# Performance work log

Hardware: AMD Instinct MI355X
Metric: run time of the kernel (lower is better)

The kernel has to match this reference:

```python
import jax, jax.numpy as jnp
import numpy as np

N_NODES = 50000
N_EDGES = 1600000
IN_DIM = 128
HID = 64
HEADS = 4
N_GRAPHS = 64
OUT_DIM = 10
NEG_SLOPE = 0.2  # PyG GATConv default leaky_relu slope


def _glorot(key, shape):
    fan_in = shape[0] if len(shape) > 1 else shape[-1]
    return jax.random.normal(key, shape, dtype=jnp.float32) / np.sqrt(fan_in)


def setup_inputs() -> dict:
    key = jax.random.key(0)
    ks = jax.random.split(key, 24)
    imgs = jax.random.normal(ks[0], (N_NODES, IN_DIM), dtype=jnp.float32)
    edge_index = jax.random.randint(ks[1], (2, N_EDGES), 0, N_NODES, dtype=jnp.int32)
    batch = jnp.sort(jax.random.randint(ks[2], (N_NODES,), 0, N_GRAPHS, dtype=jnp.int32))
    HC = HID * HEADS
    inp = {
        'imgs': imgs, 'edge_index': edge_index, 'batch': batch,
        # superpixel aggregator: Linear(input_dim, hidden)
        'W_agg': _glorot(ks[3], (IN_DIM, HID)), 'b_agg': jnp.zeros((HID,), jnp.float32),
        # GAT layer 0: hidden -> heads*hidden, concat
        'W0': _glorot(ks[4], (HID, HC)), 'as0': _glorot(ks[5], (HEADS, HID)), 'ad0': _glorot(ks[6], (HEADS, HID)), 'b0': jnp.zeros((HC,), jnp.float32),
        # GAT layer 1: heads*hidden -> heads*hidden, concat
        'W1': _glorot(ks[7], (HC, HC)), 'as1': _glorot(ks[8], (HEADS, HID)), 'ad1': _glorot(ks[9], (HEADS, HID)), 'b1': jnp.zeros((HC,), jnp.float32),
        # GAT layer 2: heads*hidden -> hidden, mean over heads
        'W2': _glorot(ks[10], (HC, HC)), 'as2': _glorot(ks[11], (HEADS, HID)), 'ad2': _glorot(ks[12], (HEADS, HID)), 'b2': jnp.zeros((HID,), jnp.float32),
        # MLP: hidden -> hidden -> out
        'mW1': _glorot(ks[13], (HID, HID)), 'mb1': jnp.zeros((HID,), jnp.float32),
        'mW2': _glorot(ks[14], (HID, OUT_DIM)), 'mb2': jnp.zeros((OUT_DIM,), jnp.float32),
    }
    return inp


def _gat_conv(x, src, dst, W, a_src, a_dst, b, concat):
    # PyG GATConv: linear -> per-head scores -> leaky_relu -> segment softmax over dst -> scatter-add
    N = x.shape[0]
    H, C = a_src.shape
    h = (x @ W).reshape(N, H, C)                      # [N,H,C]
    es = jnp.sum(h * a_src, axis=-1)                  # [N,H]
    ed = jnp.sum(h * a_dst, axis=-1)                  # [N,H]
    e = jax.nn.leaky_relu(es[src] + ed[dst], NEG_SLOPE)  # [E,H]
    m = jax.ops.segment_max(e, dst, num_segments=N)
    m = jnp.where(jnp.isfinite(m), m, 0.0)
    ex = jnp.exp(e - m[dst])                          # [E,H]
    s = jax.ops.segment_sum(ex, dst, num_segments=N)
    alpha = ex / (s[dst] + 1e-16)                     # [E,H]
    out = jax.ops.segment_sum(h[src] * alpha[..., None], dst, num_segments=N)  # [N,H,C]
    out = out.reshape(N, H * C) if concat else out.mean(axis=1)
    return out + b


def _forward(imgs, edge_index, batch, W_agg, b_agg, W0, as0, ad0, b0, W1, as1, ad1, b1, W2, as2, ad2, b2, mW1, mb1, mW2, mb2):
    N = imgs.shape[0]
    # add self loops (PyG GATConv default add_self_loops=True)
    loop = jnp.arange(N, dtype=edge_index.dtype)
    src = jnp.concatenate([edge_index[0], loop])
    dst = jnp.concatenate([edge_index[1], loop])
    x = imgs @ W_agg + b_agg                          # lrgb aggregator
    x = jax.nn.elu(_gat_conv(x, src, dst, W0, as0, ad0, b0, True))
    x = jax.nn.elu(_gat_conv(x, src, dst, W1, as1, ad1, b1, True))
    x = _gat_conv(x, src, dst, W2, as2, ad2, b2, False)
    # global mean pool over graphs
    sums = jax.ops.segment_sum(x, batch, num_segments=N_GRAPHS)
    cnt = jax.ops.segment_sum(jnp.ones((N,), x.dtype), batch, num_segments=N_GRAPHS)
    pooled = sums / jnp.maximum(cnt, 1.0)[:, None]
    # MLP (dropout inactive at inference)
    hmlp = jax.nn.relu(pooled @ mW1 + mb1)
    return hmlp @ mW2 + mb2


def reference(imgs, edge_index, batch, W_agg, b_agg, W0, as0, ad0, b0, W1, as1, ad1, b1, W2, as2, ad2, b2, mW1, mb1, mW2, mb2):
    return _forward(imgs, edge_index, batch, W_agg, b_agg, W0, as0, ad0, b0, W1, as1, ad1, b1, W2, as2, ad2, b2, mW1, mb1, mW2, mb2)
```

## Files before the change

kernel.cpp:

```cpp
#include <hip/hip_runtime.h>
#include <hip/hip_bf16.h>

#define N_NODES 50000
#define N_EDGESX 1600000
#define E_TOT   (N_EDGESX + N_NODES)
#define IN_DIM 128
#define HID 64
#define HEADS 4
#define HC 256
#define N_GRAPHS 64
#define OUT_DIM 10
#define NEG_SLOPE 0.2f

#define NBUK 196
#define CAP 12288
#define BT 4096

typedef __attribute__((ext_vector_type(8))) short bf16x8;
typedef __attribute__((ext_vector_type(4))) float f32x4;

__device__ __forceinline__ float lrelu(float x){ return fmaxf(x, NEG_SLOPE*x); }
__device__ __forceinline__ float sel4(float4 v, int i){
  float r = v.x;
  r = (i==1) ? v.y : r;
  r = (i==2) ? v.z : r;
  r = (i==3) ? v.w : r;
  return r;
}
__device__ __forceinline__ unsigned short f2bf(float f){
  union { __hip_bfloat16 b; unsigned short u; } cv;
  cv.b = __float2bfloat16(f);
  return cv.u;
}
__device__ __forceinline__ float bflo(unsigned int u){ return __uint_as_float(u << 16); }
__device__ __forceinline__ float bfhi(unsigned int u){ return __uint_as_float(u & 0xffff0000u); }

__global__ __launch_bounds__(256) void bin_k(const int* __restrict__ ei,
                                             int* __restrict__ bucket_cursor,
                                             unsigned int* __restrict__ bucket_buf){
  __shared__ unsigned int pk[BT];
  __shared__ unsigned int binned[BT];
  __shared__ int hist[256], excl[256], gbase[256], lcur[256], tmp[256];
  const int tid = threadIdx.x;
  const int e0 = blockIdx.x * BT;
  const int nv = min(BT, E_TOT - e0);
  hist[tid] = 0;
  __syncthreads();
  for (int i = tid; i < nv; i += 256){
    int e = e0 + i;
    int src, dst;
    if (e < N_EDGESX){ src = ei[e]; dst = ei[N_EDGESX + e]; }
    else { src = e - N_EDGESX; dst = src; }
    pk[i] = ((unsigned)src << 16) | (unsigned)dst;
    atomicAdd(&hist[dst >> 8], 1);
  }
  __syncthreads();
  int v = hist[tid];
  tmp[tid] = v;
  __syncthreads();
  for (int off = 1; off < 256; off <<= 1){
    int t = (tid >= off) ? tmp[tid-off] : 0;
    __syncthreads();
    tmp[tid] += t;
    __syncthreads();
  }
  excl[tid] = tmp[tid] - v;
  lcur[tid] = tmp[tid] - v;
  if (tid < NBUK && v > 0) gbase[tid] = atomicAdd(&bucket_cursor[tid], v);
  __syncthreads();
  for (int i = tid; i < nv; i += 256){
    unsigned u = pk[i];
    int b = (int)((u & 0xFFFFu) >> 8);
    int p = atomicAdd(&lcur[b], 1);
    binned[p] = u;
  }
  __syncthreads();
  for (int j = tid; j < nv; j += 256){
    unsigned u = binned[j];
    int b = (int)((u & 0xFFFFu) >> 8);
    bucket_buf[(size_t)b*CAP + gbase[b] + (j - excl[b])] = u;
  }
}

__global__ __launch_bounds__(256) void bucket_scan_k(const int* __restrict__ bucket_cursor,
                                                     int* __restrict__ bucket_base,
                                                     int* __restrict__ row_start){
  __shared__ int tmp[256];
  int t = threadIdx.x;
  int v = (t < NBUK) ? bucket_cursor[t] : 0;
  tmp[t] = v;
  __syncthreads();
  for (int off = 1; off < 256; off <<= 1){
    int x = (t >= off) ? tmp[t-off] : 0;
    __syncthreads();
    tmp[t] += x;
    __syncthreads();
  }
  if (t < NBUK) bucket_base[t] = tmp[t] - v;
  if (t == 0) row_start[N_NODES] = E_TOT;
}

__global__ __launch_bounds__(256) void build_k(const unsigned int* __restrict__ bucket_buf,
                                               const int* __restrict__ bucket_cursor,
                                               const int* __restrict__ bucket_base,
                                               int* __restrict__ row_start,
                                               int* __restrict__ csr_src){
  __shared__ int hist[256], excl[256], lcur[256], tmp[256];
  const int b = blockIdx.x;
  const int t = threadIdx.x;
  const int cntb = bucket_cursor[b];
  const int base = bucket_base[b];
  const unsigned int* buf = bucket_buf + (size_t)b*CAP;
  hist[t] = 0;
  __syncthreads();
  for (int i = t; i < cntb; i += 256) atomicAdd(&hist[buf[i] & 255], 1);
  __syncthreads();
  int v = hist[t];
  tmp[t] = v;
  __syncthreads();
  for (int off = 1; off < 256; off <<= 1){
    int x = (t >= off) ? tmp[t-off] : 0;
    __syncthreads();
    tmp[t] += x;
    __syncthreads();
  }
  excl[t] = tmp[t] - v;
  lcur[t] = tmp[t] - v;
  int g = b*256 + t;
  if (g < N_NODES) row_start[g] = base + excl[t];
  __syncthreads();
  for (int i = t; i < cntb; i += 256){
    unsigned u = buf[i];
    int p = atomicAdd(&lcur[u & 255], 1);
    csr_src[base + p] = (int)(u >> 16);
  }
}

__global__ __launch_bounds__(256) void wcvt_k(const float* __restrict__ W, unsigned short* __restrict__ WT, int K){
  int idx = blockIdx.x*256 + threadIdx.x;
  if (idx >= K*256) return;
  int k = idx >> 8, c = idx & 255;
  WT[c*K + k] = f2bf(W[k*256 + c]);
}

__global__ __launch_bounds__(256) void wproj_k(const float* __restrict__ W0,
    const float* __restrict__ as0, const float* __restrict__ ad0,
    float* __restrict__ ws0, float* __restrict__ wd0){
  int t = threadIdx.x;
  int h = t >> 6, k = t & 63;
  float s = 0.f, d = 0.f;
  for (int c = 0; c < 64; c++){
    float wv = W0[k*256 + h*64 + c];
    s = fmaf(wv, as0[h*64 + c], s);
    d = fmaf(wv, ad0[h*64 + c], d);
  }
  ws0[t] = s; wd0[t] = d;
}

__global__ __launch_bounds__(256) void agg_lin(const float* __restrict__ imgs, const float* __restrict__ W,
                                               const float* __restrict__ b,
                                               const float* __restrict__ ws0, const float* __restrict__ wd0,
                                               unsigned short* __restrict__ x0,
                                               float* __restrict__ es, float* __restrict__ ed){
  __shared__ __align__(16) float xr[4][IN_DIM];
  int w = threadIdx.x >> 6, lane = threadIdx.x & 63;
  int n = blockIdx.x*4 + w;
  if (n >= N_NODES) return;
  ((float2*)xr[w])[lane] = ((const float2*)(imgs + (size_t)n*IN_DIM))[lane];
  float acc = b[lane];
  #pragma unroll 8
  for (int k = 0; k < IN_DIM; k++)
    acc = fmaf(xr[w][k], W[k*HID + lane], acc);
  x0[(size_t)n*HID + lane] = f2bf(acc);
  float p[4], q[4];
  #pragma unroll
  for (int h = 0; h < 4; h++){
    p[h] = acc * ws0[h*64 + lane];
    q[h] = acc * wd0[h*64 + lane];
  }
  #pragma unroll
  for (int off = 32; off >= 1; off >>= 1){
    #pragma unroll
    for (int h = 0; h < 4; h++){
      p[h] += __shfl_xor(p[h], off);
      q[h] += __shfl_xor(q[h], off);
    }
  }
  if (lane == 0){
    float4 pv; pv.x=p[0]; pv.y=p[1]; pv.z=p[2]; pv.w=p[3];
    float4 qv; qv.x=q[0]; qv.y=q[1]; qv.z=q[2]; qv.w=q[3];
    *(float4*)(es + n*4) = pv;
    *(float4*)(ed + n*4) = qv;
  }
}

__global__ __launch_bounds__(256) void gat_agg0(const unsigned short* __restrict__ x0,
    const float* __restrict__ es, const float* __restrict__ ed,
    const int* __restrict__ row_start, const int* __restrict__ csr_src,
    unsigned short* __restrict__ y4){
  __shared__ int   sbuf[4][64];
  __shared__ float wbuf[4][64][4];
  const int lane = threadIdx.x & 63;
  const int wid  = threadIdx.x >> 6;
  const int n = blockIdx.x*4 + wid;
  if (n >= N_NODES) return;
  const int rs = row_start[n], re = row_start[n+1];
  const float4 edn = *(const float4*)(ed + n*4);
  const int slot = lane >> 3;
  const int f8   = lane & 7;
  float4 sumw = make_float4(0.f,0.f,0.f,0.f);
  float acc[4][8];
  #pragma unroll
  for (int h=0;h<4;h++)
    #pragma unroll
    for (int q2=0;q2<8;q2++) acc[h][q2]=0.f;

  for (int base = rs; base < re; base += 64){
    const int cl = min(64, re - base);
    int e = base + lane;
    int s = (e < re) ? csr_src[e] : 0;
    float4 e4 = *(const float4*)(es + (s<<2));
    float w0 = __expf(lrelu(e4.x + edn.x));
    float w1 = __expf(lrelu(e4.y + edn.y));
    float w2 = __expf(lrelu(e4.z + edn.z));
    float w3 = __expf(lrelu(e4.w + edn.w));
    if (e >= re){ w0=0.f; w1=0.f; w2=0.f; w3=0.f; }
    sumw.x += w0; sumw.y += w1; sumw.z += w2; sumw.w += w3;
    sbuf[wid][lane] = s;
    float4 wv; wv.x=w0; wv.y=w1; wv.z=w2; wv.w=w3;
    *(float4*)wbuf[wid][lane] = wv;
    for (int j = 0; j < cl; j += 8){
      int jj = j + slot;
      if (jj < cl){
        float4 aw = *(const float4*)wbuf[wid][jj];
        int s2 = sbuf[wid][jj];
        uint4 hv = *(const uint4*)(x0 + (((size_t)s2)<<6) + (f8<<3));
        float f[8] = {bflo(hv.x),bfhi(hv.x),bflo(hv.y),bfhi(hv.y),
                      bflo(hv.z),bfhi(hv.z),bflo(hv.w),bfhi(hv.w)};
        #pragma unroll
        for (int q2=0;q2<8;q2++){
          acc[0][q2] = fmaf(aw.x, f[q2], acc[0][q2]);
          acc[1][q2] = fmaf(aw.y, f[q2], acc[1][q2]);
          acc[2][q2] = fmaf(aw.z, f[q2], acc[2][q2]);
          acc[3][q2] = fmaf(aw.w, f[q2], acc[3][q2]);
        }
      }
    }
  }
  #pragma unroll
  for (int off = 8; off <= 32; off <<= 1){
    #pragma unroll
    for (int h=0;h<4;h++)
      #pragma unroll
      for (int q2=0;q2<8;q2++) acc[h][q2] += __shfl_xor(acc[h][q2], off);
  }
  #pragma unroll
  for (int off = 32; off >= 1; off >>= 1){
    sumw.x += __shfl_xor(sumw.x, off);
    sumw.y += __shfl_xor(sumw.y, off);
    sumw.z += __shfl_xor(sumw.z, off);
    sumw.w += __shfl_xor(sumw.w, off);
  }
  if (lane < 32){
    int h = lane >> 3;
    float inv = 1.f / (sel4(sumw, h) + 1e-16f);
    union { unsigned short u[8]; uint4 v; } ob;
    #pragma unroll
    for (int q2=0;q2<8;q2++) ob.u[q2] = f2bf(acc[h][q2] * inv);
    *(uint4*)(y4 + (size_t)n*HC + lane*8) = ob.v;
  }
}

__global__ __launch_bounds__(256) void hgemm_k(const unsigned short* __restrict__ y4,
                                               const unsigned short* __restrict__ WT0,
                                               const float* __restrict__ b0,
                                               unsigned short* __restrict__ x1){
  __shared__ __align__(16) unsigned short xs[16][264];
  const int tid = threadIdx.x;
  const int lane = tid & 63;
  const int w = tid >> 6;
  const int n0 = blockIdx.x * 16;
  for (int i = tid; i < 16*32; i += 256){
    int r = i >> 5, cc = (i & 31) * 8;
    *(uint4*)(&xs[r][cc]) = *(const uint4*)(y4 + (size_t)(n0+r)*HC + cc);
  }
  __syncthreads();
  const int g = lane >> 4, cl = lane & 15;
  f32x4 acc[4];
  #pragma unroll
  for (int c = 0; c < 4; c++) acc[c] = (f32x4){0.f,0.f,0.f,0.f};
  #pragma unroll
  for (int t = 0; t < 2; t++){
    bf16x8 a = *(const bf16x8*)(&xs[cl][w*64 + t*32 + g*8]);
    #pragma unroll
    for (int c = 0; c < 4; c++){
      bf16x8 bv = *(const bf16x8*)(WT0 + (size_t)(w*64 + c*16 + cl)*64 + t*32 + g*8);
      acc[c] = __builtin_amdgcn_mfma_f32_16x16x32_bf16(a, bv, acc[c], 0, 0, 0);
    }
  }
  #pragma unroll
  for (int c = 0; c < 4; c++){
    int col = w*64 + c*16 + cl;
    float bb = b0[col];
    #pragma unroll
    for (int j = 0; j < 4; j++){
      float v = acc[c][j] + bb;
      v = v > 0.f ? v : expm1f(v);
      x1[(size_t)(n0 + g*4 + j)*HC + col] = f2bf(v);
    }
  }
}

template<int K>
__global__ __launch_bounds__(256) void lin_mfma(const unsigned short* __restrict__ x,
                                                const unsigned short* __restrict__ WT,
                                                const float* __restrict__ as_, const float* __restrict__ ad_,
                                                unsigned short* __restrict__ hh,
                                                float* __restrict__ es, float* __restrict__ ed){
  constexpr int KP = K + 8;
  __shared__ __align__(16) unsigned short xs[16][KP];
  const int tid = threadIdx.x;
  const int lane = tid & 63;
  const int w = tid >> 6;
  const int n0 = blockIdx.x * 16;
  constexpr int CH = K/8;
  for (int i = tid; i < 16*CH; i += 256){
    int r = i / CH, cc = (i % CH)*8;
    *(uint4*)(&xs[r][cc]) = *(const uint4*)(x + (size_t)(n0+r)*K + cc);
  }
  __syncthreads();
  const int g  = lane >> 4;
  const int cl = lane & 15;
  f32x4 acc[4];
  #pragma unroll
  for (int c = 0; c < 4; c++) acc[c] = (f32x4){0.f,0.f,0.f,0.f};
  #pragma unroll
  for (int t = 0; t < K/32; t++){
    bf16x8 a = *(const bf16x8*)(&xs[cl][t*32 + g*8]);
    #pragma unroll
    for (int c = 0; c < 4; c++){
      bf16x8 bv = *(const bf16x8*)(WT + (size_t)(w*64 + c*16 + cl)*K + t*32 + g*8);
      acc[c] = __builtin_amdgcn_mfma_f32_16x16x32_bf16(a, bv, acc[c], 0, 0, 0);
    }
  }
  float pes[4] = {0.f,0.f,0.f,0.f}, ped[4] = {0.f,0.f,0.f,0.f};
  #pragma unroll
  for (int c = 0; c < 4; c++){
    float av = as_[w*64 + c*16 + cl];
    float dv = ad_[w*64 + c*16 + cl];
    #pragma unroll
    for (int j = 0; j < 4; j++){
      pes[j] = fmaf(acc[c][j], av, pes[j]);
      ped[j] = fmaf(acc[c][j], dv, ped[j]);
    }
  }
  #pragma unroll
  for (int off = 8; off >= 1; off >>= 1){
    #pragma unroll
    for (int j = 0; j < 4; j++){
      pes[j] += __shfl_xor(pes[j], off);
      ped[j] += __shfl_xor(ped[j], off);
    }
  }
  if (cl == 0){
    #pragma unroll
    for (int j = 0; j < 4; j++){
      int n = n0 + g*4 + j;
      es[n*4 + w] = pes[j];
      ed[n*4 + w] = ped[j];
    }
  }
  #pragma unroll
  for (int c = 0; c < 4; c++){
    #pragma unroll
    for (int j = 0; j < 4; j++){
      hh[((size_t)w*N_NODES + (n0 + g*4 + j))*HID + c*16 + cl] = f2bf(acc[c][j]);
    }
  }
}

template<int ACT, int OBF>
__global__ __launch_bounds__(256) void gat_agg_h(const unsigned short* __restrict__ hh,
    const float* __restrict__ es, const float* __restrict__ ed,
    const int* __restrict__ row_start, const int* __restrict__ csr_src,
    const float* __restrict__ bias, void* __restrict__ outp){
  __shared__ int   sbuf[4][64];
  __shared__ float wbuf[4][64];
  const int lane = threadIdx.x & 63;
  const int wid  = threadIdx.x >> 6;
  const int hy   = blockIdx.y;
  const int n = blockIdx.x*4 + wid;
  if (n >= N_NODES) return;
  const int rs = row_start[n], re = row_start[n+1];
  const float edh = ed[n*4 + hy];
  const int slot = lane >> 3;
  const int f8   = lane & 7;
  const unsigned short* __restrict__ tab = hh + (((size_t)hy * N_NODES) << 6);
  float sumw = 0.f;
  float acc[8];
  #pragma unroll
  for (int q2=0;q2<8;q2++) acc[q2]=0.f;

  for (int base = rs; base < re; base += 64){
    const int cl = min(64, re - base);
    int e = base + lane;
    int s = (e < re) ? csr_src[e] : 0;
    float w = (e < re) ? __expf(lrelu(es[(s<<2)+hy] + edh)) : 0.f;
    sumw += w;
    sbuf[wid][lane] = s;
    wbuf[wid][lane] = w;
    for (int j = 0; j < cl; j += 8){
      int jj = j + slot;
      if (jj < cl){
        float a = wbuf[wid][jj];
        int s2 = sbuf[wid][jj];
        uint4 hv = *(const uint4*)(tab + (((size_t)s2)<<6) + (f8<<3));
        acc[0] = fmaf(a, bflo(hv.x), acc[0]);
        acc[1] = fmaf(a, bfhi(hv.x), acc[1]);
        acc[2] = fmaf(a, bflo(hv.y), acc[2]);
        acc[3] = fmaf(a, bfhi(hv.y), acc[3]);
        acc[4] = fmaf(a, bflo(hv.z), acc[4]);
        acc[5] = fmaf(a, bfhi(hv.z), acc[5]);
        acc[6] = fmaf(a, bflo(hv.w), acc[6]);
        acc[7] = fmaf(a, bfhi(hv.w), acc[7]);
      }
    }
  }
  #pragma unroll
  for (int off = 8; off <= 32; off <<= 1){
    #pragma unroll
    for (int q2=0;q2<8;q2++) acc[q2] += __shfl_xor(acc[q2], off);
  }
  #pragma unroll
  for (int off = 32; off >= 1; off >>= 1) sumw += __shfl_xor(sumw, off);
  const float inv = 1.f / (sumw + 1e-16f);
  float o[8];
  #pragma unroll
  for (int q2=0;q2<8;q2++) o[q2] = acc[q2]*inv;
  if (ACT){
    #pragma unroll
    for (int q2=0;q2<8;q2++){
      float v = o[q2] + bias[hy*64 + f8*8 + q2];
      o[q2] = v > 0.f ? v : expm1f(v);
    }
  }
  if (lane < 8){
    if (OBF){
      union { unsigned short u[8]; uint4 v; } ob;
      #pragma unroll
      for (int q2=0;q2<8;q2++) ob.u[q2] = f2bf(o[q2]);
      *(uint4*)((unsigned short*)outp + (size_t)n*HC + hy*64 + lane*8) = ob.v;
    } else {
      float* dst = (float*)outp + (size_t)n*HC + hy*64 + lane*8;
      float4 v0; v0.x=o[0]; v0.y=o[1]; v0.z=o[2]; v0.w=o[3];
      float4 v1; v1.x=o[4]; v1.y=o[5]; v1.z=o[6]; v1.w=o[7];
      *(float4*)dst = v0;
      *(float4*)(dst+4) = v1;
    }
  }
}

#define PB_NODES 128
__global__ __launch_bounds__(256) void pool_k(const float* __restrict__ xagg,
                                              const int* __restrict__ batch, float* __restrict__ pooled,
                                              float* __restrict__ cnt){
  int c = threadIdx.x & 63;
  int sub = threadIdx.x >> 6;
  int n0 = blockIdx.x * PB_NODES;
  int nend = n0 + PB_NODES; if (nend > N_NODES) nend = N_NODES;
  float acc = 0.f; int curg = -1; int cl = 0;
  for (int n = n0 + sub; n < nend; n += 4){
    int g = batch[n];
    if (g != curg){
      if (curg >= 0){
        unsafeAtomicAdd(pooled + curg*HID + c, acc);
        if (c == 0) unsafeAtomicAdd(cnt + curg, (float)cl);
      }
      curg = g; acc = 0.f; cl = 0;
    }
    const float* r = xagg + (size_t)n*HC;
    acc += 0.25f*(r[c] + r[64+c] + r[128+c] + r[192+c]);
    cl++;
  }
  if (curg >= 0){
    unsafeAtomicAdd(pooled + curg*HID + c, acc);
    if (c == 0) unsafeAtomicAdd(cnt + curg, (float)cl);
  }
}

__global__ __launch_bounds__(64) void mlp_k(const float* __restrict__ pooled, const float* __restrict__ cnt,
                                            const float* __restrict__ b2,
                                            const float* __restrict__ mW1, const float* __restrict__ mb1,
                                            const float* __restrict__ mW2, const float* __restrict__ mb2,
                                            float* __restrict__ out){
  __shared__ float p[HID], h1[HID];
  int g = blockIdx.x, j = threadIdx.x;
  float c = fmaxf(cnt[g], 1.f);
  p[j] = pooled[g*HID + j] / c + b2[j];
  __syncthreads();
  float acc = mb1[j];
  #pragma unroll 8
  for (int k = 0; k < HID; k++) acc = fmaf(p[k], mW1[k*HID + j], acc);
  h1[j] = fmaxf(acc, 0.f);
  __syncthreads();
  if (j < OUT_DIM){
    float a2 = mb2[j];
    #pragma unroll 8
    for (int k = 0; k < HID; k++) a2 = fmaf(h1[k], mW2[k*OUT_DIM + j], a2);
    out[g*OUT_DIM + j] = a2;
  }
}

extern "C" void kernel_launch(void* const* d_in, const int* in_sizes, int n_in,
                              void* d_out, int out_size, void* d_ws, size_t ws_size,
                              hipStream_t stream){
  const float* imgs  = (const float*)d_in[0];
  const int*   ei    = (const int*)d_in[1];
  const int*   batch = (const int*)d_in[2];
  const float* W_agg = (const float*)d_in[3];
  const float* b_agg = (const float*)d_in[4];
  const float* W0 = (const float*)d_in[5];
  const float* as0 = (const float*)d_in[6];
  const float* ad0 = (const float*)d_in[7];
  const float* b0 = (const float*)d_in[8];
  const float* W1 = (const float*)d_in[9];
  const float* as1 = (const float*)d_in[10];
  const float* ad1 = (const float*)d_in[11];
  const float* b1 = (const float*)d_in[12];
  const float* W2 = (const float*)d_in[13];
  const float* as2 = (const float*)d_in[14];
  const float* ad2 = (const float*)d_in[15];
  const float* b2 = (const float*)d_in[16];
  const float* mW1 = (const float*)d_in[17];
  const float* mb1 = (const float*)d_in[18];
  const float* mW2 = (const float*)d_in[19];
  const float* mb2 = (const float*)d_in[20];
  float* out = (float*)d_out;

  float* xf32 = (float*)d_ws;
  unsigned short* y4 = (unsigned short*)xf32;
  unsigned short* hb  = (unsigned short*)(xf32 + (size_t)N_NODES*HC);
  unsigned short* xbf = hb + (size_t)N_NODES*HC;
  float* es   = (float*)(xbf + (size_t)N_NODES*HC);
  float* ed   = es + (size_t)N_NODES*HEADS;
  float* pooled = ed + (size_t)N_NODES*HEADS;
  float* cnt  = pooled + N_GRAPHS*HID;
  float* ws0  = cnt + N_GRAPHS;
  float* wd0  = ws0 + 256;
  int* row_start = (int*)(wd0 + 256);
  int* csr_src   = row_start + (N_NODES+1);
  int* bucket_cursor = csr_src + E_TOT;
  int* bucket_base   = bucket_cursor + NBUK;
  unsigned short* WT0 = (unsigned short*)(bucket_base + NBUK);
  unsigned short* WT1 = WT0 + 256*64;
  unsigned short* WT2 = WT1 + 256*256;
  unsigned int* bucket_buf = (unsigned int*)(WT2 + 256*256);
  unsigned short* x0bf = (unsigned short*)bucket_buf;

  hipMemsetAsync(bucket_cursor, 0, NBUK*sizeof(int), stream);
  bin_k<<<(E_TOT + BT - 1)/BT, 256, 0, stream>>>(ei, bucket_cursor, bucket_buf);
  bucket_scan_k<<<1, 256, 0, stream>>>(bucket_cursor, bucket_base, row_start);
  build_k<<<NBUK, 256, 0, stream>>>(bucket_buf, bucket_cursor, bucket_base, row_start, csr_src);

  wcvt_k<<<(64*256+255)/256, 256, 0, stream>>>(W0, WT0, 64);
  wcvt_k<<<(256*256+255)/256, 256, 0, stream>>>(W1, WT1, 256);
  wcvt_k<<<(256*256+255)/256, 256, 0, stream>>>(W2, WT2, 256);
  wproj_k<<<1, 256, 0, stream>>>(W0, as0, ad0, ws0, wd0);

  const int MB = N_NODES/16;
  const int GB = (N_NODES + 3)/4;
  dim3 GH(GB, HEADS, 1);

  agg_lin<<<GB, 256, 0, stream>>>(imgs, W_agg, b_agg, ws0, wd0, x0bf, es, ed);

  gat_agg0<<<GB, 256, 0, stream>>>(x0bf, es, ed, row_start, csr_src, y4);
  hgemm_k<<<MB, 256, 0, stream>>>(y4, WT0, b0, xbf);

  lin_mfma<256><<<MB, 256, 0, stream>>>(xbf, WT1, as1, ad1, hb, es, ed);
  gat_agg_h<1,1><<<GH, 256, 0, stream>>>(hb, es, ed, row_start, csr_src, b1, xbf);

  lin_mfma<256><<<MB, 256, 0, stream>>>(xbf, WT2, as2, ad2, hb, es, ed);
  gat_agg_h<0,0><<<GH, 256, 0, stream>>>(hb, es, ed, row_start, csr_src, nullptr, xf32);

  hipMemsetAsync(pooled, 0, (N_GRAPHS*HID + N_GRAPHS)*sizeof(float), stream);
  pool_k<<<(N_NODES + PB_NODES - 1)/PB_NODES, 256, 0, stream>>>(xf32, batch, pooled, cnt);
  mlp_k<<<N_GRAPHS, 64, 0, stream>>>(pooled, cnt, b2, mW1, mb1, mW2, mb2, out);
}
```

Measured before the change: 678.1 us.

## Fuse per-head GAT aggregation into one node-major pass over all heads

The projected features move from a head-major layout ([head][node][64]) to a node-major layout ([node][256]). The aggregation kernel now processes all four heads in one wave per destination node instead of launching one block row per head. Each source row is read as one contiguous 512-byte chunk, and the CSR index and attention-score work per edge is done once instead of four times. Address arithmetic switches to 32-bit unsigned offsets. In exchange, each lane does more loads per edge iteration, and the gather footprint per edge is larger.

```diff
diff --git a/kernel.cpp b/kernel.cpp
--- a/kernel.cpp
+++ b/kernel.cpp
@@ -234,7 +234,7 @@
       if (jj < cl){
         float4 aw = *(const float4*)wbuf[wid][jj];
         int s2 = sbuf[wid][jj];
-        uint4 hv = *(const uint4*)(x0 + (((size_t)s2)<<6) + (f8<<3));
+        uint4 hv = *(const uint4*)(x0 + ((unsigned)(s2<<6) + (unsigned)(f8<<3)));
         float f[8] = {bflo(hv.x),bfhi(hv.x),bflo(hv.y),bfhi(hv.y),
                       bflo(hv.z),bfhi(hv.z),bflo(hv.w),bfhi(hv.w)};
         #pragma unroll
@@ -315,7 +315,7 @@
 __global__ __launch_bounds__(256) void lin_mfma(const unsigned short* __restrict__ x,
                                                 const unsigned short* __restrict__ WT,
                                                 const float* __restrict__ as_, const float* __restrict__ ad_,
-                                                unsigned short* __restrict__ hh,
+                                                unsigned short* __restrict__ h,
                                                 float* __restrict__ es, float* __restrict__ ed){
   constexpr int KP = K + 8;
   __shared__ __align__(16) unsigned short xs[16][KP];
@@ -374,89 +374,93 @@
   for (int c = 0; c < 4; c++){
     #pragma unroll
     for (int j = 0; j < 4; j++){
-      hh[((size_t)w*N_NODES + (n0 + g*4 + j))*HID + c*16 + cl] = f2bf(acc[c][j]);
+      h[(size_t)(n0 + g*4 + j)*HC + w*64 + c*16 + cl] = f2bf(acc[c][j]);
     }
   }
 }
 
 template<int ACT, int OBF>
-__global__ __launch_bounds__(256) void gat_agg_h(const unsigned short* __restrict__ hh,
+__global__ __launch_bounds__(256) void gat_agg(const unsigned short* __restrict__ h,
     const float* __restrict__ es, const float* __restrict__ ed,
     const int* __restrict__ row_start, const int* __restrict__ csr_src,
     const float* __restrict__ bias, void* __restrict__ outp){
   __shared__ int   sbuf[4][64];
-  __shared__ float wbuf[4][64];
+  __shared__ float wbuf[4][64][4];
   const int lane = threadIdx.x & 63;
   const int wid  = threadIdx.x >> 6;
-  const int hy   = blockIdx.y;
   const int n = blockIdx.x*4 + wid;
   if (n >= N_NODES) return;
   const int rs = row_start[n], re = row_start[n+1];
-  const float edh = ed[n*4 + hy];
-  const int slot = lane >> 3;
-  const int f8   = lane & 7;
-  const unsigned short* __restrict__ tab = hh + (((size_t)hy * N_NODES) << 6);
-  float sumw = 0.f;
-  float acc[8];
-  #pragma unroll
-  for (int q2=0;q2<8;q2++) acc[q2]=0.f;
+  const float4 edn = *(const float4*)(ed + n*4);
+  const int half = lane >> 5;
+  const int l5   = lane & 31;
+  const int hh   = l5 >> 3;
+  const unsigned voff_lane = (unsigned)(l5 << 3);
+
+  float4 sum4 = make_float4(0.f,0.f,0.f,0.f);
+  float a0=0.f,a1=0.f,a2=0.f,a3=0.f,a4=0.f,a5=0.f,a6=0.f,a7=0.f;
 
   for (int base = rs; base < re; base += 64){
     const int cl = min(64, re - base);
     int e = base + lane;
     int s = (e < re) ? csr_src[e] : 0;
-    float w = (e < re) ? __expf(lrelu(es[(s<<2)+hy] + edh)) : 0.f;
-    sumw += w;
+    float4 e4 = *(const float4*)(es + (s<<2));
+    float w0 = __expf(lrelu(e4.x + edn.x));
+    float w1 = __expf(lrelu(e4.y + edn.y));
+    float w2 = __expf(lrelu(e4.z + edn.z));
+    float w3 = __expf(lrelu(e4.w + edn.w));
+    if (e >= re){ w0=0.f; w1=0.f; w2=0.f; w3=0.f; }
+    sum4.x += w0; sum4.y += w1; sum4.z += w2; sum4.w += w3;
     sbuf[wid][lane] = s;
-    wbuf[wid][lane] = w;
-    for (int j = 0; j < cl; j += 8){
-      int jj = j + slot;
-      if (jj < cl){
-        float a = wbuf[wid][jj];
-        int s2 = sbuf[wid][jj];
-        uint4 hv = *(const uint4*)(tab + (((size_t)s2)<<6) + (f8<<3));
-        acc[0] = fmaf(a, bflo(hv.x), acc[0]);
-        acc[1] = fmaf(a, bfhi(hv.x), acc[1]);
-        acc[2] = fmaf(a, bflo(hv.y), acc[2]);
-        acc[3] = fmaf(a, bfhi(hv.y), acc[3]);
-        acc[4] = fmaf(a, bflo(hv.z), acc[4]);
-        acc[5] = fmaf(a, bfhi(hv.z), acc[5]);
-        acc[6] = fmaf(a, bflo(hv.w), acc[6]);
-        acc[7] = fmaf(a, bfhi(hv.w), acc[7]);
-      }
-    }
-  }
-  #pragma unroll
-  for (int off = 8; off <= 32; off <<= 1){
-    #pragma unroll
-    for (int q2=0;q2<8;q2++) acc[q2] += __shfl_xor(acc[q2], off);
-  }
-  #pragma unroll
-  for (int off = 32; off >= 1; off >>= 1) sumw += __shfl_xor(sumw, off);
-  const float inv = 1.f / (sumw + 1e-16f);
-  float o[8];
-  #pragma unroll
-  for (int q2=0;q2<8;q2++) o[q2] = acc[q2]*inv;
+    float4 wv4; wv4.x=w0; wv4.y=w1; wv4.z=w2; wv4.w=w3;
+    *(float4*)wbuf[wid][lane] = wv4;
+    for (int j = 0; j < cl; j += 2){
+      int jj = j + half;
+      float a  = wbuf[wid][jj][hh];
+      int   s2 = sbuf[wid][jj];
+      uint4 hv = *(const uint4*)(h + ((unsigned)(s2<<8) + voff_lane));
+      a0 = fmaf(a, bflo(hv.x), a0);
+      a1 = fmaf(a, bfhi(hv.x), a1);
+      a2 = fmaf(a, bflo(hv.y), a2);
+      a3 = fmaf(a, bfhi(hv.y), a3);
+      a4 = fmaf(a, bflo(hv.z), a4);
+      a5 = fmaf(a, bfhi(hv.z), a5);
+      a6 = fmaf(a, bflo(hv.w), a6);
+      a7 = fmaf(a, bfhi(hv.w), a7);
+    }
+  }
+  #pragma unroll
+  for (int off = 32; off >= 1; off >>= 1){
+    sum4.x += __shfl_xor(sum4.x, off);
+    sum4.y += __shfl_xor(sum4.y, off);
+    sum4.z += __shfl_xor(sum4.z, off);
+    sum4.w += __shfl_xor(sum4.w, off);
+  }
+  const float inv = 1.f / (sel4(sum4, hh) + 1e-16f);
+  a0 += __shfl_xor(a0, 32); a1 += __shfl_xor(a1, 32);
+  a2 += __shfl_xor(a2, 32); a3 += __shfl_xor(a3, 32);
+  a4 += __shfl_xor(a4, 32); a5 += __shfl_xor(a5, 32);
+  a6 += __shfl_xor(a6, 32); a7 += __shfl_xor(a7, 32);
+  float4 o;
+  o.x = (half ? a4 : a0) * inv;
+  o.y = (half ? a5 : a1) * inv;
+  o.z = (half ? a6 : a2) * inv;
+  o.w = (half ? a7 : a3) * inv;
+  const int fbase = l5*8 + half*4;
   if (ACT){
-    #pragma unroll
-    for (int q2=0;q2<8;q2++){
-      float v = o[q2] + bias[hy*64 + f8*8 + q2];
-      o[q2] = v > 0.f ? v : expm1f(v);
-    }
-  }
-  if (lane < 8){
-    if (OBF){
-      union { unsigned short u[8]; uint4 v; } ob;
-      #pragma unroll
-      for (int q2=0;q2<8;q2++) ob.u[q2] = f2bf(o[q2]);
-      *(uint4*)((unsigned short*)outp + (size_t)n*HC + hy*64 + lane*8) = ob.v;
-    } else {
-      float* dst = (float*)outp + (size_t)n*HC + hy*64 + lane*8;
-      float4 v0; v0.x=o[0]; v0.y=o[1]; v0.z=o[2]; v0.w=o[3];
-      float4 v1; v1.x=o[4]; v1.y=o[5]; v1.z=o[6]; v1.w=o[7];
-      *(float4*)dst = v0;
-      *(float4*)(dst+4) = v1;
-    }
+    float4 b4 = *(const float4*)(bias + fbase);
+    o.x += b4.x; o.y += b4.y; o.z += b4.z; o.w += b4.w;
+    o.x = o.x > 0.f ? o.x : expm1f(o.x);
+    o.y = o.y > 0.f ? o.y : expm1f(o.y);
+    o.z = o.z > 0.f ? o.z : expm1f(o.z);
+    o.w = o.w > 0.f ? o.w : expm1f(o.w);
+  }
+  if (OBF){
+    ushort4 ob;
+    ob.x = f2bf(o.x); ob.y = f2bf(o.y); ob.z = f2bf(o.z); ob.w = f2bf(o.w);
+    *(ushort4*)((unsigned short*)outp + (size_t)n*HC + fbase) = ob;
+  } else {
+    *(float4*)((float*)outp + (size_t)n*HC + fbase) = o;
   }
 }
 
@@ -569,7 +573,6 @@
 
   const int MB = N_NODES/16;
   const int GB = (N_NODES + 3)/4;
-  dim3 GH(GB, HEADS, 1);
 
   agg_lin<<<GB, 256, 0, stream>>>(imgs, W_agg, b_agg, ws0, wd0, x0bf, es, ed);
 
@@ -577,10 +580,10 @@
   hgemm_k<<<MB, 256, 0, stream>>>(y4, WT0, b0, xbf);
 
   lin_mfma<256><<<MB, 256, 0, stream>>>(xbf, WT1, as1, ad1, hb, es, ed);
-  gat_agg_h<1,1><<<GH, 256, 0, stream>>>(hb, es, ed, row_start, csr_src, b1, xbf);
+  gat_agg<1,1><<<GB, 256, 0, stream>>>(hb, es, ed, row_start, csr_src, b1, xbf);
 
   lin_mfma<256><<<MB, 256, 0, stream>>>(xbf, WT2, as2, ad2, hb, es, ed);
-  gat_agg_h<0,0><<<GH, 256, 0, stream>>>(hb, es, ed, row_start, csr_src, nullptr, xf32);
+  gat_agg<0,0><<<GB, 256, 0, stream>>>(hb, es, ed, row_start, csr_src, nullptr, xf32);
 
   hipMemsetAsync(pooled, 0, (N_GRAPHS*HID + N_GRAPHS)*sizeof(float), stream);
   pool_k<<<(N_NODES + PB_NODES - 1)/PB_NODES, 256, 0, stream>>>(xf32, batch, pooled, cnt);
```

Result: faster. 612.5 us (-9.7%).
